# Performance work log

Measured on AMD Instinct MI355X. Metric: run time of the kernel, lower is better.

Reference implementation:

```python
import jax, jax.numpy as jnp
import numpy as np

HEAD_DIM = 64

def rotate_half(x):
    x1, x2 = jnp.split(x, 2, axis=-1)
    return jnp.concatenate([-x2, x1], axis=-1)

def setup_inputs() -> dict:
    key = jax.random.key(0)
    ks = jax.random.split(key, 6)
    B, T, E = 1, 2048, 2048
    H, KV, D = 32, 8, HEAD_DIM
    BS, W = 64, 256
    hidden_states = jax.random.normal(ks[0], (B, T, E), jnp.float32)
    Wq = jax.random.normal(ks[1], (H * D, E), jnp.float32) / np.float32(np.sqrt(E))
    Wk = jax.random.normal(ks[2], (KV * D, E), jnp.float32) / np.float32(np.sqrt(E))
    Wv = jax.random.normal(ks[3], (KV * D, E), jnp.float32) / np.float32(np.sqrt(E))
    Wo = jax.random.normal(ks[4], (E, H * D), jnp.float32) / np.float32(np.sqrt(H * D))
    # RoPE tables (Llama-style, theta=10000)
    pos = jnp.arange(T, dtype=jnp.float32)
    inv_freq = 1.0 / (10000.0 ** (jnp.arange(0, D, 2, dtype=jnp.float32) / D))
    freqs = pos[:, None] * inv_freq[None, :]                 # [T, D/2]
    emb = jnp.concatenate([freqs, freqs], axis=-1)           # [T, D]
    cos = jnp.cos(emb)[None]                                 # [1, T, D]
    sin = jnp.sin(emb)[None]
    rw_allow_blocks = jax.random.bernoulli(ks[5], 0.15, (B, T // BS, T // BS))
    return {"hidden_states": hidden_states, "cos": cos, "sin": sin,
            "Wq": Wq, "Wk": Wk, "Wv": Wv, "Wo": Wo,
            "rw_allow_blocks": rw_allow_blocks,
            "rw_block_size": BS, "rw_window_tokens": W}

def reference(hidden_states, cos, sin, Wq, Wk, Wv, Wo,
              rw_allow_blocks, rw_block_size, rw_window_tokens):
    B, T, E = hidden_states.shape
    D = HEAD_DIM
    H = Wq.shape[0] // D
    KV = Wk.shape[0] // D
    n_rep = H // KV  # num_key_value_groups
    scaling = D ** -0.5

    # projections -> [B, heads, T, D]
    q = (hidden_states @ Wq.T).reshape(B, T, H, D).transpose(0, 2, 1, 3)
    k = (hidden_states @ Wk.T).reshape(B, T, KV, D).transpose(0, 2, 1, 3)
    v = (hidden_states @ Wv.T).reshape(B, T, KV, D).transpose(0, 2, 1, 3)

    # rotary embedding (unsqueeze_dim=1)
    c = cos[:, None, :, :]
    s = sin[:, None, :, :]
    q = q * c + rotate_half(q) * s
    k = k * c + rotate_half(k) * s

    # repeat_kv for GQA
    k = jnp.repeat(k, n_rep, axis=1)
    v = jnp.repeat(v, n_rep, axis=1)

    scores = jnp.einsum('bhqd,bhkd->bhqk', q, k) * scaling   # [B,H,T,T]

    # expand block allow pattern to token resolution
    allow = jnp.repeat(jnp.repeat(rw_allow_blocks, rw_block_size, axis=1),
                       rw_block_size, axis=2)[:, :T, :T]     # [B,T,T]
    # causal sliding window + attention sink (first window tokens always visible)
    qi = jnp.arange(T)[:, None]
    ki = jnp.arange(T)[None, :]
    win = ((ki <= qi) & (ki >= qi - rw_window_tokens + 1)) | (ki < rw_window_tokens)
    allow = allow | win[None]

    neg = jnp.finfo(scores.dtype).min
    scores = jnp.where(allow[:, None, :, :], scores, neg)
    probs = jax.nn.softmax(scores.astype(jnp.float32), axis=-1).astype(q.dtype)

    out = jnp.einsum('bhqk,bhkd->bhqd', probs, v)            # [B,H,T,D]
    out = out.transpose(0, 2, 1, 3).reshape(B, T, H * D)
    return out @ Wo.T                                        # [B,T,E]
```

## Files before the change

kernel.cpp:

```cpp
#include <hip/hip_runtime.h>

typedef unsigned short bfu;
typedef __attribute__((ext_vector_type(8))) short short8;
typedef __attribute__((ext_vector_type(4))) float f32x4;

#define TT 2048
#define EE 2048

#define GBAR() do { __builtin_amdgcn_sched_barrier(0); \
                    __builtin_amdgcn_s_barrier();      \
                    __builtin_amdgcn_sched_barrier(0); } while (0)

__device__ __forceinline__ unsigned short f2bf(float f) {
  union { float fv; unsigned int u; } v; v.fv = f;
  unsigned int r = v.u + 0x7fffu + ((v.u >> 16) & 1u);
  return (unsigned short)(r >> 16);
}

__device__ __forceinline__ unsigned int cvtpk(float lo, float hi) {
  unsigned int r;
  asm("v_cvt_pk_bf16_f32 %0, %1, %2" : "=v"(r) : "v"(lo), "v"(hi));
  return r;
}

__device__ __forceinline__ float fexp2(float x) {
  float r;
  asm("v_exp_f32 %0, %1" : "=v"(r) : "v"(x));
  return r;
}

__device__ __forceinline__ void gload16(const void* g, void* l) {
  __builtin_amdgcn_global_load_lds(
      (const __attribute__((address_space(1))) unsigned int*)g,
      (__attribute__((address_space(3))) unsigned int*)l, 16, 0, 0);
}

__global__ __launch_bounds__(256) void cvt5(
    const float* __restrict__ s0, const float* __restrict__ s1,
    const float* __restrict__ s2, const float* __restrict__ s3,
    const float* __restrict__ s4,
    bfu* __restrict__ d0, bfu* __restrict__ d1, bfu* __restrict__ d2,
    bfu* __restrict__ d3, bfu* __restrict__ d4,
    const unsigned char* __restrict__ mask_in, unsigned char* __restrict__ mask_out) {
  if (blockIdx.y == 5) {
    if (blockIdx.x != 0) return;
    __shared__ int mis;
    if (threadIdx.x == 0) mis = 0;
    __syncthreads();
    int any = 0;
    for (int i = threadIdx.x; i < 1024; i += 256)
      if ((i & 3) != 0 && mask_in[i] != 0) any = 1;
    if (any) atomicAdd(&mis, 1);
    __syncthreads();
    for (int i = threadIdx.x; i < 1024; i += 256) {
      if (mis == 0) mask_out[i] = (((const int*)mask_in)[i] != 0) ? 1 : 0;
      else          mask_out[i] = mask_in[i] ? 1 : 0;
    }
    return;
  }
  const float* s; bfu* d; int n;
  switch (blockIdx.y) {
    case 0:  s = s0; d = d0; n = 4194304; break;
    case 1:  s = s1; d = d1; n = 4194304; break;
    case 2:  s = s2; d = d2; n = 1048576; break;
    case 3:  s = s3; d = d3; n = 1048576; break;
    default: s = s4; d = d4; n = 4194304; break;
  }
  for (int i = (blockIdx.x * 256 + threadIdx.x) * 8; i < n; i += 512 * 256 * 8) {
    float4 a = *(const float4*)(s + i);
    float4 b = *(const float4*)(s + i + 4);
    short8 pk;
    pk[0] = (short)f2bf(a.x); pk[1] = (short)f2bf(a.y);
    pk[2] = (short)f2bf(a.z); pk[3] = (short)f2bf(a.w);
    pk[4] = (short)f2bf(b.x); pk[5] = (short)f2bf(b.y);
    pk[6] = (short)f2bf(b.z); pk[7] = (short)f2bf(b.w);
    *(short8*)(d + i) = pk;
  }
}

__global__ __launch_bounds__(512) void gemm_qkv(
    const bfu* __restrict__ A, const bfu* __restrict__ Bq,
    const bfu* __restrict__ Bk, const bfu* __restrict__ Bv,
    bfu* __restrict__ qr, bfu* __restrict__ kro, bfu* __restrict__ vt,
    const float* __restrict__ cosb, const float* __restrict__ sinb, float qsc) {
  __shared__ bfu As[2][64 * 64];
  __shared__ bfu Bs[2][128 * 64];
  const int bx = blockIdx.x;
  int path, n0;
  const bfu* B;
  if (bx < 16)      { path = 0; B = Bq; n0 = bx * 128; }
  else if (bx < 20) { path = 1; B = Bk; n0 = (bx - 16) * 128; }
  else              { path = 2; B = Bv; n0 = (bx - 20) * 128; }
  const int t = threadIdx.x;
  const int wid = t >> 6, lane = t & 63;
  const int wr = wid >> 1, wc = wid & 1;
  const int lr = lane & 15, lh = lane >> 4;
  const int m0 = blockIdx.y * 64;
  const int K = EE;
  f32x4 acc[4] = {};

  const int srow = t >> 3, sslot = t & 7;
  const int browB = (t + 512) >> 3, sslotB = (t + 512) & 7;
  auto stage = [&](int buf, int k0) {
    gload16(A + (size_t)(m0 + srow) * K + k0 + ((sslot ^ (srow & 7)) * 8),
            &As[buf][wid * 512]);
    gload16(B + (size_t)(n0 + srow) * K + k0 + ((sslot ^ (srow & 7)) * 8),
            &Bs[buf][wid * 512]);
    gload16(B + (size_t)(n0 + browB) * K + k0 + ((sslotB ^ (browB & 7)) * 8),
            &Bs[buf][4096 + wid * 512]);
  };

  stage(0, 0);
  for (int kt = 0; kt < 32; ++kt) {
    const int cur = kt & 1;
    if (kt < 31) {
      stage(cur ^ 1, (kt + 1) * 64);
      asm volatile("s_waitcnt vmcnt(3)" ::: "memory");
    } else {
      asm volatile("s_waitcnt vmcnt(0)" ::: "memory");
    }
    GBAR();
    #pragma unroll
    for (int ks = 0; ks < 2; ++ks) {
      short8 a, b[4];
      a = *(const short8*)(&As[cur][(wr * 16 + lr) * 64 +
                                    (((ks * 4 + lh) ^ (lr & 7)) * 8)]);
      #pragma unroll
      for (int n = 0; n < 4; ++n)
        b[n] = *(const short8*)(&Bs[cur][(wc * 64 + n * 16 + lr) * 64 +
                                         (((ks * 4 + lh) ^ (lr & 7)) * 8)]);
      #pragma unroll
      for (int n = 0; n < 4; ++n)
        acc[n] = __builtin_amdgcn_mfma_f32_16x16x32_bf16(a, b[n], acc[n], 0, 0, 0);
    }
    GBAR();
  }
  #pragma unroll
  for (int r = 0; r < 4; ++r) {
    const int row = m0 + wr * 16 + lh * 4 + r;
    #pragma unroll
    for (int n = 0; n < 4; ++n) {
      const int col = n0 + wc * 64 + n * 16 + lr;
      float x = acc[n][r];
      if (path == 2) {
        vt[((size_t)(row >> 6) * 512 + col) * 64 + (row & 63)] = f2bf(x);
      } else {
        const int d = col & 63;
        float xp = (n < 2) ? -acc[n + 2][r] : acc[n - 2][r];
        float c = cosb[row * 64 + d], s = sinb[row * 64 + d];
        float sc = (path == 0) ? qsc : 1.0f;
        bfu* dst = (path == 0) ? qr : kro;
        dst[((size_t)(col >> 6) * TT + row) * 64 + d] = f2bf((x * c + xp * s) * sc);
      }
    }
  }
}

__global__ __launch_bounds__(512) void gemm_o(
    const bfu* __restrict__ A, const bfu* __restrict__ B,
    float* __restrict__ outF, int M, int N, int K) {
  __shared__ bfu As[2][64 * 64];
  __shared__ bfu Bs[2][128 * 64];
  const int t = threadIdx.x;
  const int wid = t >> 6, lane = t & 63;
  const int wr = wid >> 1, wc = wid & 1;
  const int lr = lane & 15, lh = lane >> 4;
  const int m0 = blockIdx.y * 64, n0 = blockIdx.x * 128;
  f32x4 acc[4] = {};

  const int srow = t >> 3, sslot = t & 7;
  const int browB = (t + 512) >> 3, sslotB = (t + 512) & 7;
  auto stage = [&](int buf, int k0) {
    gload16(A + (size_t)(m0 + srow) * K + k0 + ((sslot ^ (srow & 7)) * 8),
            &As[buf][wid * 512]);
    gload16(B + (size_t)(n0 + srow) * K + k0 + ((sslot ^ (srow & 7)) * 8),
            &Bs[buf][wid * 512]);
    gload16(B + (size_t)(n0 + browB) * K + k0 + ((sslotB ^ (browB & 7)) * 8),
            &Bs[buf][4096 + wid * 512]);
  };

  stage(0, 0);
  const int nk = K >> 6;
  for (int kt = 0; kt < nk; ++kt) {
    const int cur = kt & 1;
    if (kt < nk - 1) {
      stage(cur ^ 1, (kt + 1) * 64);
      asm volatile("s_waitcnt vmcnt(3)" ::: "memory");
    } else {
      asm volatile("s_waitcnt vmcnt(0)" ::: "memory");
    }
    GBAR();
    #pragma unroll
    for (int ks = 0; ks < 2; ++ks) {
      short8 a, b[4];
      a = *(const short8*)(&As[cur][(wr * 16 + lr) * 64 +
                                    (((ks * 4 + lh) ^ (lr & 7)) * 8)]);
      #pragma unroll
      for (int n = 0; n < 4; ++n)
        b[n] = *(const short8*)(&Bs[cur][(wc * 64 + n * 16 + lr) * 64 +
                                         (((ks * 4 + lh) ^ (lr & 7)) * 8)]);
      #pragma unroll
      for (int n = 0; n < 4; ++n)
        acc[n] = __builtin_amdgcn_mfma_f32_16x16x32_bf16(a, b[n], acc[n], 0, 0, 0);
    }
    GBAR();
  }
  #pragma unroll
  for (int r = 0; r < 4; ++r) {
    const int row = m0 + wr * 16 + lh * 4 + r;
    #pragma unroll
    for (int n = 0; n < 4; ++n)
      outF[(size_t)row * N + n0 + wc * 64 + n * 16 + lr] = acc[n][r];
  }
}

__global__ __launch_bounds__(256, 4) void attn_kernel(
    const bfu* __restrict__ qr, const bfu* __restrict__ kr,
    const bfu* __restrict__ vt, const unsigned char* __restrict__ allow,
    bfu* __restrict__ ao) {
  const int qb = blockIdx.x, h = blockIdx.y, kv = h >> 2;
  const int t = threadIdx.x, wid = t >> 6, lane = t & 63;
  const int lr = lane & 15, lh = lane >> 4;
  const int q0 = qb * 64;
  const int qrow = q0 + wid * 16 + lr;
  __shared__ bfu KB[2][64 * 64];
  __shared__ bfu VB[2][64 * 64];
  __shared__ bfu P[4][16 * 64];
  bfu* Pw = P[wid];

  unsigned int amask = 0, emask = 0;
  for (int kb = 0; kb < 32; ++kb) {
    bool bm = allow[qb * 32 + kb] != 0;
    bool fw = (kb < 4) || (kb >= qb - 3 && kb <= qb - 1);
    bool ed = (kb == qb) || (kb == qb - 4);
    if (bm || fw || ed) {
      amask |= 1u << kb;
      if (!bm && !fw) emask |= 1u << kb;
    }
  }

  short8 bq[2];
  #pragma unroll
  for (int ks = 0; ks < 2; ++ks)
    bq[ks] = *(const short8*)(qr + ((size_t)h * TT + qrow) * 64 + ks * 32 + lh * 8);

  short8 vones;
  #pragma unroll
  for (int i = 0; i < 8; ++i) vones[i] = (short)0x3F80;

  f32x4 o[4] = {};
  f32x4 o_l = {};
  float m_reg = -1e30f;

  auto stage = [&](bfu* buf, const bfu* gbase) {
    #pragma unroll
    for (int c = 0; c < 2; ++c) {
      int chunk = wid * 128 + c * 64 + lane;
      int row = chunk >> 3, s = chunk & 7;
      gload16(gbase + row * 64 + (s ^ (row & 7)) * 8,
              buf + (wid * 128 + c * 64) * 8);
    }
  };

  auto qk_tile = [&](const bfu* KBuf, int kb, f32x4 s[4]) {
    __builtin_amdgcn_s_setprio(1);
    #pragma unroll
    for (int j = 0; j < 4; ++j) {
      const int row = j * 16 + lr;
      short8 a0 = *(const short8*)(KBuf + row * 64 + ((lh    ) ^ (row & 7)) * 8);
      short8 a1 = *(const short8*)(KBuf + row * 64 + ((lh + 4) ^ (row & 7)) * 8);
      f32x4 z = {};
      z = __builtin_amdgcn_mfma_f32_16x16x32_bf16(a0, bq[0], z, 0, 0, 0);
      s[j] = __builtin_amdgcn_mfma_f32_16x16x32_bf16(a1, bq[1], z, 0, 0, 0);
    }
    __builtin_amdgcn_s_setprio(0);
    if ((emask >> kb) & 1) {
      #pragma unroll
      for (int j = 0; j < 4; ++j)
        #pragma unroll
        for (int reg = 0; reg < 4; ++reg) {
          int k = kb * 64 + j * 16 + lh * 4 + reg;
          bool ok = (k <= qrow && k >= qrow - 255) || (k < 256);
          if (!ok) s[j][reg] = -1e30f;
        }
    }
  };

  auto pv_tile = [&](const bfu* VBuf, f32x4 s[4]) {
    #pragma unroll
    for (int j = 0; j < 4; ++j) {
      unsigned int w0 = cvtpk(s[j][0], s[j][1]);
      unsigned int w1 = cvtpk(s[j][2], s[j][3]);
      int base = lr * 64 + (((j * 2 + (lh >> 1)) ^ (lr & 7)) * 8) + (lh & 1) * 4;
      *(unsigned int*)(Pw + base) = w0;
      *(unsigned int*)(Pw + base + 2) = w1;
    }
    short8 pa[2];
    #pragma unroll
    for (int ks = 0; ks < 2; ++ks)
      pa[ks] = *(const short8*)(Pw + lr * 64 + (((ks * 4 + lh) ^ (lr & 7)) * 8));
    __builtin_amdgcn_s_setprio(1);
    #pragma unroll
    for (int n = 0; n < 4; ++n) {
      #pragma unroll
      for (int ks = 0; ks < 2; ++ks) {
        const int row = n * 16 + lr;
        short8 bv = *(const short8*)(VBuf + row * 64 + ((ks * 4 + lh) ^ (row & 7)) * 8);
        o[n] = __builtin_amdgcn_mfma_f32_16x16x32_bf16(pa[ks], bv, o[n], 0, 0, 0);
      }
    }
    o_l = __builtin_amdgcn_mfma_f32_16x16x32_bf16(pa[0], vones, o_l, 0, 0, 0);
    o_l = __builtin_amdgcn_mfma_f32_16x16x32_bf16(pa[1], vones, o_l, 0, 0, 0);
    __builtin_amdgcn_s_setprio(0);
  };

  unsigned int am = amask;
  while (am) {
    const int k1 = __ffs(am) - 1; am &= am - 1;
    int k2 = -1;
    if (am) { k2 = __ffs(am) - 1; am &= am - 1; }

    __syncthreads();
    stage(KB[0], kr + ((size_t)kv * TT + k1 * 64) * 64);
    stage(VB[0], vt + ((size_t)k1 * 512 + kv * 64) * 64);
    if (k2 >= 0) {
      stage(KB[1], kr + ((size_t)kv * TT + k2 * 64) * 64);
      stage(VB[1], vt + ((size_t)k2 * 512 + kv * 64) * 64);
    }
    __syncthreads();

    f32x4 s1[4], s2[4];
    qk_tile(KB[0], k1, s1);
    if (k2 >= 0) qk_tile(KB[1], k2, s2);

    float mx = fmaxf(fmaxf(s1[0][0], s1[0][1]), fmaxf(s1[0][2], s1[0][3]));
    #pragma unroll
    for (int j = 1; j < 4; ++j)
      mx = fmaxf(mx, fmaxf(fmaxf(s1[j][0], s1[j][1]), fmaxf(s1[j][2], s1[j][3])));
    if (k2 >= 0) {
      #pragma unroll
      for (int j = 0; j < 4; ++j)
        mx = fmaxf(mx, fmaxf(fmaxf(s2[j][0], s2[j][1]), fmaxf(s2[j][2], s2[j][3])));
    }
    mx = fmaxf(mx, __shfl_xor(mx, 16));
    mx = fmaxf(mx, __shfl_xor(mx, 32));

    if (__any(mx > m_reg)) {
      float mnew = fmaxf(m_reg, mx);
      float corr = fexp2(m_reg - mnew);
      m_reg = mnew;
      #pragma unroll
      for (int r = 0; r < 4; ++r) {
        float cr = __shfl(corr, lh * 4 + r);
        #pragma unroll
        for (int n = 0; n < 4; ++n) o[n][r] *= cr;
        o_l[r] *= cr;
      }
    }

    #pragma unroll
    for (int j = 0; j < 4; ++j)
      #pragma unroll
      for (int reg = 0; reg < 4; ++reg)
        s1[j][reg] = fexp2(s1[j][reg] - m_reg);
    if (k2 >= 0) {
      #pragma unroll
      for (int j = 0; j < 4; ++j)
        #pragma unroll
        for (int reg = 0; reg < 4; ++reg)
          s2[j][reg] = fexp2(s2[j][reg] - m_reg);
    }

    pv_tile(VB[0], s1);
    if (k2 >= 0) pv_tile(VB[1], s2);
  }

  #pragma unroll
  for (int r = 0; r < 4; ++r) {
    float inv = 1.0f / o_l[r];
    #pragma unroll
    for (int n = 0; n < 4; ++n) {
      float val = o[n][r] * inv;
      ao[(size_t)(q0 + wid * 16 + lh * 4 + r) * EE + h * 64 + n * 16 + lr] = f2bf(val);
    }
  }
}

extern "C" void kernel_launch(void* const* d_in, const int* in_sizes, int n_in,
                              void* d_out, int out_size, void* d_ws, size_t ws_size,
                              hipStream_t stream) {
  const float* hs   = (const float*)d_in[0];
  const float* cosb = (const float*)d_in[1];
  const float* sinb = (const float*)d_in[2];
  const float* Wq   = (const float*)d_in[3];
  const float* Wk   = (const float*)d_in[4];
  const float* Wv   = (const float*)d_in[5];
  const float* Wo   = (const float*)d_in[6];
  const unsigned char* allow_raw = (const unsigned char*)d_in[7];
  float* out = (float*)d_out;

  char* ws = (char*)d_ws;
  const size_t MB = 1024 * 1024;
  bfu* hsb = (bfu*)(ws);
  bfu* wqb = (bfu*)(ws + 8 * MB);
  bfu* wkb = (bfu*)(ws + 16 * MB);
  bfu* wvb = (bfu*)(ws + 18 * MB);
  bfu* wob = (bfu*)(ws + 20 * MB);
  bfu* qr  = (bfu*)(ws + 28 * MB);
  bfu* kr  = (bfu*)(ws + 36 * MB);
  bfu* vt  = (bfu*)(ws + 38 * MB);
  unsigned char* maskc = (unsigned char*)(ws + 40 * MB);
  bfu* ao = hsb;

  cvt5<<<dim3(512, 6), 256, 0, stream>>>(hs, Wq, Wk, Wv, Wo,
                                         hsb, wqb, wkb, wvb, wob,
                                         allow_raw, maskc);

  const float QSC = 0.125f * 1.44269504088896f;
  gemm_qkv<<<dim3(24, 32), 512, 0, stream>>>(
      hsb, wqb, wkb, wvb, qr, kr, vt, cosb, sinb, QSC);

  attn_kernel<<<dim3(32, 32), 256, 0, stream>>>(qr, kr, vt, maskc, ao);

  gemm_o<<<dim3(16, 32), 512, 0, stream>>>(ao, wob, out, 2048, 2048, 2048);
}
```

Before: 122.2 us.

## Process one KV block per iteration to cut LDS and raise occupancy

Removes the two-block batching in the sparse attention loop, so each iteration stages, scores and accumulates a single K/V tile. This halves the K/V shared-memory buffers and register pressure, and the launch bound is raised to allow 6 blocks per CU. The cost is twice as many barrier-separated iterations with less memory-level parallelism per block, which the higher occupancy is meant to hide.

```diff
diff --git a/kernel.cpp b/kernel.cpp
--- a/kernel.cpp
+++ b/kernel.cpp
@@ -214,7 +214,7 @@
   }
 }
 
-__global__ __launch_bounds__(256, 4) void attn_kernel(
+__global__ __launch_bounds__(256, 6) void attn_kernel(
     const bfu* __restrict__ qr, const bfu* __restrict__ kr,
     const bfu* __restrict__ vt, const unsigned char* __restrict__ allow,
     bfu* __restrict__ ao) {
@@ -223,8 +223,8 @@
   const int lr = lane & 15, lh = lane >> 4;
   const int q0 = qb * 64;
   const int qrow = q0 + wid * 16 + lr;
-  __shared__ bfu KB[2][64 * 64];
-  __shared__ bfu VB[2][64 * 64];
+  __shared__ bfu KB[64 * 64];
+  __shared__ bfu VB[64 * 64];
   __shared__ bfu P[4][16 * 64];
   bfu* Pw = P[wid];
 
@@ -317,31 +317,19 @@
   unsigned int am = amask;
   while (am) {
     const int k1 = __ffs(am) - 1; am &= am - 1;
-    int k2 = -1;
-    if (am) { k2 = __ffs(am) - 1; am &= am - 1; }
 
     __syncthreads();
-    stage(KB[0], kr + ((size_t)kv * TT + k1 * 64) * 64);
-    stage(VB[0], vt + ((size_t)k1 * 512 + kv * 64) * 64);
-    if (k2 >= 0) {
-      stage(KB[1], kr + ((size_t)kv * TT + k2 * 64) * 64);
-      stage(VB[1], vt + ((size_t)k2 * 512 + kv * 64) * 64);
-    }
+    stage(KB, kr + ((size_t)kv * TT + k1 * 64) * 64);
+    stage(VB, vt + ((size_t)k1 * 512 + kv * 64) * 64);
     __syncthreads();
 
-    f32x4 s1[4], s2[4];
-    qk_tile(KB[0], k1, s1);
-    if (k2 >= 0) qk_tile(KB[1], k2, s2);
+    f32x4 s1[4];
+    qk_tile(KB, k1, s1);
 
     float mx = fmaxf(fmaxf(s1[0][0], s1[0][1]), fmaxf(s1[0][2], s1[0][3]));
     #pragma unroll
     for (int j = 1; j < 4; ++j)
       mx = fmaxf(mx, fmaxf(fmaxf(s1[j][0], s1[j][1]), fmaxf(s1[j][2], s1[j][3])));
-    if (k2 >= 0) {
-      #pragma unroll
-      for (int j = 0; j < 4; ++j)
-        mx = fmaxf(mx, fmaxf(fmaxf(s2[j][0], s2[j][1]), fmaxf(s2[j][2], s2[j][3])));
-    }
     mx = fmaxf(mx, __shfl_xor(mx, 16));
     mx = fmaxf(mx, __shfl_xor(mx, 32));
 
@@ -363,16 +351,8 @@
       #pragma unroll
       for (int reg = 0; reg < 4; ++reg)
         s1[j][reg] = fexp2(s1[j][reg] - m_reg);
-    if (k2 >= 0) {
-      #pragma unroll
-      for (int j = 0; j < 4; ++j)
-        #pragma unroll
-        for (int reg = 0; reg < 4; ++reg)
-          s2[j][reg] = fexp2(s2[j][reg] - m_reg);
-    }
-
-    pv_tile(VB[0], s1);
-    if (k2 >= 0) pv_tile(VB[1], s2);
+
+    pv_tile(VB, s1);
   }
 
   #pragma unroll
```

After: 125.5 us. +2.7%, slower.

## Overlap Wo bf16 conversion with attention and reverse query-block order

Applied to the files above, without the earlier changes.

The Wo fp32-to-bf16 conversion moves out of the upfront conversion kernel and into 32 extra blocks of the attention grid, so it runs alongside attention instead of ahead of the QKV GEMM. Attention query blocks are now issued in reverse order so the heavier late-query blocks, which see more allowed key blocks, get scheduled first and load balance better. The conversion blocks compete with attention for bandwidth and CUs. With only 32 conversion blocks, each has a long loop, which could leave a tail.

```diff
diff --git a/kernel.cpp b/kernel.cpp
--- a/kernel.cpp
+++ b/kernel.cpp
@@ -38,11 +38,10 @@
 __global__ __launch_bounds__(256) void cvt5(
     const float* __restrict__ s0, const float* __restrict__ s1,
     const float* __restrict__ s2, const float* __restrict__ s3,
-    const float* __restrict__ s4,
     bfu* __restrict__ d0, bfu* __restrict__ d1, bfu* __restrict__ d2,
-    bfu* __restrict__ d3, bfu* __restrict__ d4,
+    bfu* __restrict__ d3,
     const unsigned char* __restrict__ mask_in, unsigned char* __restrict__ mask_out) {
-  if (blockIdx.y == 5) {
+  if (blockIdx.y == 4) {
     if (blockIdx.x != 0) return;
     __shared__ int mis;
     if (threadIdx.x == 0) mis = 0;
@@ -63,8 +62,7 @@
     case 0:  s = s0; d = d0; n = 4194304; break;
     case 1:  s = s1; d = d1; n = 4194304; break;
     case 2:  s = s2; d = d2; n = 1048576; break;
-    case 3:  s = s3; d = d3; n = 1048576; break;
-    default: s = s4; d = d4; n = 4194304; break;
+    default: s = s3; d = d3; n = 1048576; break;
   }
   for (int i = (blockIdx.x * 256 + threadIdx.x) * 8; i < n; i += 512 * 256 * 8) {
     float4 a = *(const float4*)(s + i);
@@ -217,8 +215,23 @@
 __global__ __launch_bounds__(256, 4) void attn_kernel(
     const bfu* __restrict__ qr, const bfu* __restrict__ kr,
     const bfu* __restrict__ vt, const unsigned char* __restrict__ allow,
-    bfu* __restrict__ ao) {
-  const int qb = blockIdx.x, h = blockIdx.y, kv = h >> 2;
+    bfu* __restrict__ ao,
+    const float* __restrict__ WoF, bfu* __restrict__ wob) {
+  if (blockIdx.y == 32) {
+    for (int i = (blockIdx.x * 256 + threadIdx.x) * 8; i < 4194304; i += 32 * 256 * 8) {
+      float4 a = *(const float4*)(WoF + i);
+      float4 b = *(const float4*)(WoF + i + 4);
+      short8 pk;
+      pk[0] = (short)f2bf(a.x); pk[1] = (short)f2bf(a.y);
+      pk[2] = (short)f2bf(a.z); pk[3] = (short)f2bf(a.w);
+      pk[4] = (short)f2bf(b.x); pk[5] = (short)f2bf(b.y);
+      pk[6] = (short)f2bf(b.z); pk[7] = (short)f2bf(b.w);
+      *(short8*)(wob + i) = pk;
+    }
+    return;
+  }
+  const int qb = 31 - blockIdx.x;
+  const int h = blockIdx.y, kv = h >> 2;
   const int t = threadIdx.x, wid = t >> 6, lane = t & 63;
   const int lr = lane & 15, lh = lane >> 4;
   const int q0 = qb * 64;
@@ -412,15 +425,15 @@
   unsigned char* maskc = (unsigned char*)(ws + 40 * MB);
   bfu* ao = hsb;
 
-  cvt5<<<dim3(512, 6), 256, 0, stream>>>(hs, Wq, Wk, Wv, Wo,
-                                         hsb, wqb, wkb, wvb, wob,
+  cvt5<<<dim3(512, 5), 256, 0, stream>>>(hs, Wq, Wk, Wv,
+                                         hsb, wqb, wkb, wvb,
                                          allow_raw, maskc);
 
   const float QSC = 0.125f * 1.44269504088896f;
   gemm_qkv<<<dim3(24, 32), 512, 0, stream>>>(
       hsb, wqb, wkb, wvb, qr, kr, vt, cosb, sinb, QSC);
 
-  attn_kernel<<<dim3(32, 32), 256, 0, stream>>>(qr, kr, vt, maskc, ao);
+  attn_kernel<<<dim3(32, 33), 256, 0, stream>>>(qr, kr, vt, maskc, ao, Wo, wob);
 
   gemm_o<<<dim3(16, 32), 512, 0, stream>>>(ao, wob, out, 2048, 2048, 2048);
 }
```

Result: slower. 129.1 us (+5.6%).
